# Performance work log

Measured on AMD Instinct MI355X. Metric: run time of the kernel, lower is better.

The kernel has to match this reference:

```python
import jax, jax.numpy as jnp
import numpy as np

N = 4096    # channels * n = 4 * 1024
N_IN = 1024
FC = 512


def ldr_layer(x, G, H, subd_A, subd_B, bias):
    """y = W x + bias, where W = sum_i K(A, g_i) K(B, h_i)^T and A, B are
    subdiagonal matrices with entries subd_A, subd_B (Krylov LDR fast multiply).

    Closed form: K(A, g)[i, j] = g[i-j] * c[i] / c[i-j] for i >= j (0 otherwise),
    with c = [1, cumprod(subd_A)]. This turns the multiply into FFT
    correlations/convolutions of length 2n instead of a dense n x n GEMM.
    x: (b, n); G, H: (r, n); subd_A, subd_B: (n-1,); bias: (n,).
    """
    n = x.shape[-1]
    one = jnp.ones((1,), x.dtype)
    c = jnp.concatenate([one, jnp.cumprod(subd_A)])   # (n,) cumulative subdiag products of A
    d = jnp.concatenate([one, jnp.cumprod(subd_B)])   # (n,)
    L = 2 * n
    q = H / d                                          # (r, n)
    gp = G / c                                         # (r, n)
    p = x * d                                          # (b, n)
    # u[b, r, j] = (K(B, h_r)^T x)[j] = sum_k q[r, k] * p[b, j + k]  (cross-correlation)
    Fp = jnp.fft.rfft(p, n=L)                          # (b, n+1)
    Fq = jnp.fft.rfft(q, n=L)                          # (r, n+1)
    u = jnp.fft.irfft(Fp[:, None] * jnp.conj(Fq)[None], n=L)[..., :n]  # (b, r, n)
    # out[b, i] = c[i] * sum_r (gp_r * u[b, r])_conv[i]  (causal convolution)
    Fg = jnp.fft.rfft(gp, n=L)                         # (r, n+1)
    Fu = jnp.fft.rfft(u, n=L)                          # (b, r, n+1)
    out = jnp.fft.irfft(jnp.einsum('rk,brk->bk', Fg, Fu), n=L)[:, :n]
    return c * out + bias


def setup_inputs() -> dict:
    key = jax.random.key(0)
    ks = jax.random.split(key, 14)
    std = 0.01  # params.init_stddev
    f32 = jnp.float32
    inp = {
        'x': jax.random.normal(ks[0], (128, N_IN), f32),
        'G1': std * jax.random.normal(ks[1], (48, N), f32),
        'H1': std * jax.random.normal(ks[2], (48, N), f32),
        'subd_A1': jnp.exp(0.01 * jax.random.normal(ks[3], (N - 1,), f32)),
        'subd_B1': jnp.exp(0.01 * jax.random.normal(ks[4], (N - 1,), f32)),
        'b1': std * jax.random.normal(ks[5], (N,), f32),
        'G2': std * jax.random.normal(ks[6], (16, N), f32),
        'H2': std * jax.random.normal(ks[7], (16, N), f32),
        'subd_A2': jnp.exp(0.01 * jax.random.normal(ks[8], (N - 1,), f32)),
        'subd_B2': jnp.exp(0.01 * jax.random.normal(ks[9], (N - 1,), f32)),
        'b2': std * jax.random.normal(ks[10], (N,), f32),
        'W_logits': jax.random.normal(ks[11], (10, FC), f32) / np.sqrt(FC).astype(np.float32),
        'b_logits': std * jax.random.normal(ks[12], (10,), f32),
    }
    return inp


def reference(x, G1, H1, subd_A1, subd_B1, b1, G2, H2, subd_A2, subd_B2, b2,
              W_logits, b_logits):
    bsz, n_in = x.shape
    xp = jnp.concatenate([x, jnp.zeros((bsz, N - n_in), x.dtype)], axis=-1)  # pad to channels*n
    h = jax.nn.relu(ldr_layer(xp, G1, H1, subd_A1, subd_B1, b1))
    h = jax.nn.relu(ldr_layer(h, G2, H2, subd_A2, subd_B2, b2))
    return h[:, :FC] @ W_logits.T + b_logits
```

## Files before the change

### kernel.cpp

```cpp
#include <hip/hip_runtime.h>
#include <hip/hip_bf16.h>

#define BATCH 128
#define NIN   1024
#define NFULL 4096
#define R1    48
#define R2    16
#define FCDIM 512
#define NOUT  10

#define WS_C1  0
#define WS_D1  4096
#define WS_C2  8192
#define WS_D2  12288
#define WS_P1  16384
#define WS_P2  (WS_P1 + BATCH*NIN)
#define WS_PT1 (WS_P2 + BATCH*NFULL)
#define WS_P2M (WS_PT1 + NIN*NFULL)
#define WS_CT1 (WS_P2M + FCDIM*NFULL)
#define WS_CT2 (WS_CT1 + 32*5120)
#define WS_VP1 (WS_CT2 + 16*4608)
#define WS_VP2 (WS_VP1 + 4*BATCH*NFULL)
#define WS_END (WS_VP2 + 32*BATCH*FCDIM)

#define NCH1 32
#define NCH2 16
#define CHROWS 32
#define CTLD1 5120
#define CTLD2 4608

typedef __attribute__((ext_vector_type(8))) short bf16x8;
typedef __attribute__((ext_vector_type(4))) float f32x4;

__device__ __forceinline__ unsigned short f2b(float f) {
    unsigned u = __builtin_bit_cast(unsigned, f);
    return (unsigned short)((u + 0x7fffu + ((u >> 16) & 1u)) >> 16);
}
__device__ __forceinline__ float b2f(unsigned short h) {
    unsigned u = ((unsigned)h) << 16;
    return __builtin_bit_cast(float, u);
}
#define MFMA16(a, b, c) __builtin_amdgcn_mfma_f32_16x16x32_bf16(a, b, c, 0, 0, 0)

__global__ void __launch_bounds__(256) prep_fused(
    const float* __restrict__ x, const float* __restrict__ sA1,
    const float* __restrict__ sB1, const float* __restrict__ sA2,
    const float* __restrict__ sB2, float* __restrict__ ws) {
    __shared__ float cd[4096];
    __shared__ float tot[256];
    int b = blockIdx.x, t = threadIdx.x;
    const float* src = (b == 0) ? sA1 : (b == 1) ? sB1 : (b == 2) ? sA2
                      : (b == 3) ? sB2 : sB1;
    float loc[16];
    float prod = 1.f;
#pragma unroll
    for (int u = 0; u < 16; ++u) {
        int idx = t * 16 + u;
        float e = (idx == 0) ? 1.f : src[idx - 1];
        prod *= e;
        loc[u] = prod;
    }
    tot[t] = prod;
    __syncthreads();
    for (int off = 1; off < 256; off <<= 1) {
        float v = (t >= off) ? tot[t - off] : 1.f;
        __syncthreads();
        tot[t] *= v;
        __syncthreads();
    }
    float excl = (t == 0) ? 1.f : tot[t - 1];
#pragma unroll
    for (int u = 0; u < 16; ++u) cd[t * 16 + u] = excl * loc[u];
    __syncthreads();

    if (b < 4) {
        float* dst = ws + (size_t)b * 4096;
#pragma unroll
        for (int u = 0; u < 16; ++u) { int i = t + u * 256; dst[i] = cd[i]; }
    } else {
        unsigned short* p1h = (unsigned short*)(ws + WS_P1);
        unsigned short* p1l = p1h + BATCH * NIN;
        int row0 = (b - 4) * 4;
#pragma unroll
        for (int u = 0; u < 16; ++u) {
            int lin = t + u * 256;
            int row = row0 + (lin >> 10), col = lin & 1023;
            float f = x[(size_t)row * NIN + col] * cd[col];
            unsigned short h = f2b(f);
            p1h[(size_t)row * NIN + col] = h;
            p1l[(size_t)row * NIN + col] = f2b(f - b2f(h));
        }
    }
}

__global__ void __launch_bounds__(256) gemm_rank_kernel(
    const float* __restrict__ H1, const float* __restrict__ G1,
    const float* __restrict__ G2, const float* __restrict__ H2,
    float* __restrict__ ws) {
    const int which = blockIdx.z;
    if (which == 1 && blockIdx.y >= 8) return;
    const float* A    = which == 0 ? H1 : G2;
    const float* B    = which == 0 ? G1 : H2;
    const float* divA = ws + (which == 0 ? WS_D1 : WS_C2);
    const float* divB = ws + (which == 0 ? WS_C1 : WS_D2);
    float* C          = ws + (which == 0 ? WS_PT1 : WS_P2M);
    const int Kr      = which == 0 ? R1 : R2;
    __shared__ float As[R1 * 68];
    __shared__ float Bs[R1 * 68];
    int tid = threadIdx.x;
    int tx = tid & 15, ty = tid >> 4;
    int n0 = blockIdx.x * 64;
    int m0 = blockIdx.y * 64;
    int nf4 = Kr * 16;
    for (int lin = tid; lin < nf4; lin += 256) {
        int r = lin >> 4, i4 = lin & 15;
        float4 va = *(const float4*)&A[(size_t)r * NFULL + m0 + i4 * 4];
        float4 da = *(const float4*)&divA[m0 + i4 * 4];
        va.x /= da.x; va.y /= da.y; va.z /= da.z; va.w /= da.w;
        *(float4*)&As[r * 68 + i4 * 4] = va;
        float4 vb = *(const float4*)&B[(size_t)r * NFULL + n0 + i4 * 4];
        float4 db = *(const float4*)&divB[n0 + i4 * 4];
        vb.x /= db.x; vb.y /= db.y; vb.z /= db.z; vb.w /= db.w;
        *(float4*)&Bs[r * 68 + i4 * 4] = vb;
    }
    __syncthreads();
    float acc[4][4] = {};
#pragma unroll 8
    for (int r = 0; r < Kr; ++r) {
        float4 a4 = *(const float4*)&As[r * 68 + ty * 4];
        float4 b4 = *(const float4*)&Bs[r * 68 + tx * 4];
        acc[0][0] += a4.x * b4.x; acc[0][1] += a4.x * b4.y;
        acc[0][2] += a4.x * b4.z; acc[0][3] += a4.x * b4.w;
        acc[1][0] += a4.y * b4.x; acc[1][1] += a4.y * b4.y;
        acc[1][2] += a4.y * b4.z; acc[1][3] += a4.y * b4.w;
        acc[2][0] += a4.z * b4.x; acc[2][1] += a4.z * b4.y;
        acc[2][2] += a4.z * b4.z; acc[2][3] += a4.z * b4.w;
        acc[3][0] += a4.w * b4.x; acc[3][1] += a4.w * b4.y;
        acc[3][2] += a4.w * b4.z; acc[3][3] += a4.w * b4.w;
    }
#pragma unroll
    for (int i = 0; i < 4; ++i) {
        int m = m0 + ty * 4 + i;
        *(float4*)&C[(size_t)m * NFULL + n0 + tx * 4] =
            make_float4(acc[i][0], acc[i][1], acc[i][2], acc[i][3]);
    }
}

__global__ void diag_scan_p1(float* __restrict__ ws) {
    const int which = blockIdx.z;
    const int nch   = which == 0 ? NCH1 : NCH2;
    if (blockIdx.y >= (unsigned)nch) return;
    float* P        = ws + (which == 0 ? WS_PT1 : WS_P2M);
    float* ctot     = ws + (which == 0 ? WS_CT1 : WS_CT2);
    const int R     = which == 0 ? NIN : FCDIM;
    const int nd    = R + NFULL - 1;
    const int ctld  = which == 0 ? CTLD1 : CTLD2;
    int t = blockIdx.x * 256 + threadIdx.x;
    if (t >= nd) return;
    int doff = t - (R - 1);
    int z = blockIdx.y;
    int m0 = z * CHROWS;
    int mlo = max(m0, -doff);
    int mhi = min(m0 + CHROWS, min(NFULL - doff, R));
    float run = 0.f;
    if (mlo < mhi) {
        float* p = P + (size_t)mlo * NFULL + (mlo + doff);
        const size_t step = NFULL + 1;
        int len = mhi - mlo;
        int s = 0;
        for (; s + 16 <= len; s += 16) {
            float v[16];
#pragma unroll
            for (int u = 0; u < 16; ++u) v[u] = p[u * step];
#pragma unroll
            for (int u = 0; u < 16; ++u) { run += v[u]; v[u] = run; }
#pragma unroll
            for (int u = 0; u < 16; ++u) p[u * step] = v[u];
            p += 16 * step;
        }
        for (; s < len; ++s) { float v = *p; run += v; *p = run; p += step; }
    }
    ctot[(size_t)z * ctld + t] = run;
}

__global__ void off_prefix(float* __restrict__ ws) {
    const int which = blockIdx.z;
    float* ct      = ws + (which == 0 ? WS_CT1 : WS_CT2);
    const int ctld = which == 0 ? CTLD1 : CTLD2;
    const int nch  = which == 0 ? NCH1 : NCH2;
    int t = blockIdx.x * 256 + threadIdx.x;
    if (t >= ctld) return;
    float run = 0.f;
    for (int z = 0; z < nch; ++z) {
        float v = ct[(size_t)z * ctld + t];
        ct[(size_t)z * ctld + t] = run;
        run += v;
    }
}

#define L1_LOADA(H0, H1, L0, L1v, KS) { \
    int kk_ = kbase + (KS) * 32 + 8 * g; \
    const unsigned short* pa_ = p1h + (size_t)(mq * 32 + lm) * NIN + kk_; \
    const unsigned short* pb_ = p1l + (size_t)(mq * 32 + lm) * NIN + kk_; \
    H0 = *(const bf16x8*)pa_;  H1 = *(const bf16x8*)(pa_ + 16 * NIN); \
    L0 = *(const bf16x8*)pb_;  L1v = *(const bf16x8*)(pb_ + 16 * NIN); }

#define L1_LOADS(KS) { \
    int kg_ = kbase + (KS) * 32 + 2 * k2; \
    const float* pr_ = P1 + (size_t)kg_ * NFULL + n0 + 2 * n2; \
    float2 va_ = *(const float2*)pr_; \
    float2 vb_ = *(const float2*)(pr_ + NFULL); \
    const float* orow_ = OFF1 + (size_t)(kg_ >> 5) * CTLD1 + (1023 + n0 + 2 * n2 - kg_); \
    float om_ = orow_[-1], oc_ = orow_[0], op_ = orow_[1]; \
    f00 = va_.x + oc_; f01 = va_.y + op_; f10 = vb_.x + om_; f11 = vb_.y + oc_; }

#define L1_WRITES() { \
    unsigned short h00_ = f2b(f00), h10_ = f2b(f10), h01_ = f2b(f01), h11_ = f2b(f11); \
    int a0_ = (2 * n2) * 20 + k2; \
    Bh[a0_]      = (unsigned)h00_ | ((unsigned)h10_ << 16); \
    Bh[a0_ + 20] = (unsigned)h01_ | ((unsigned)h11_ << 16); \
    Bl[a0_]      = (unsigned)f2b(f00 - b2f(h00_)) | ((unsigned)f2b(f10 - b2f(h10_)) << 16); \
    Bl[a0_ + 20] = (unsigned)f2b(f01 - b2f(h01_)) | ((unsigned)f2b(f11 - b2f(h11_)) << 16); }

#define L1_COMPUTE(H0, H1, L0, L1v) { \
    int nb_ = (nh * 32 + lm) * 20 + 4 * g; \
    uint4 uh0_ = *(const uint4*)&Bh[nb_];       uint4 ul0_ = *(const uint4*)&Bl[nb_]; \
    uint4 uh1_ = *(const uint4*)&Bh[nb_ + 320]; uint4 ul1_ = *(const uint4*)&Bl[nb_ + 320]; \
    bf16x8 bh0_ = __builtin_bit_cast(bf16x8, uh0_), bl0_ = __builtin_bit_cast(bf16x8, ul0_); \
    bf16x8 bh1_ = __builtin_bit_cast(bf16x8, uh1_), bl1_ = __builtin_bit_cast(bf16x8, ul1_); \
    acc00 = MFMA16(H0, bh0_, acc00); acc10 = MFMA16(H1, bh0_, acc10); \
    acc01 = MFMA16(H0, bh1_, acc01); acc11 = MFMA16(H1, bh1_, acc11); \
    acc00 = MFMA16(H0, bl0_, acc00); acc10 = MFMA16(H1, bl0_, acc10); \
    acc01 = MFMA16(H0, bl1_, acc01); acc11 = MFMA16(H1, bl1_, acc11); \
    acc00 = MFMA16(L0, bh0_, acc00); acc10 = MFMA16(L1v, bh0_, acc10); \
    acc01 = MFMA16(L0, bh1_, acc01); acc11 = MFMA16(L1v, bh1_, acc11); }

#define L1_STEP(CH0, CH1, CL0, CL1, NH0, NH1, NL0, NL1, KS, LAST) \
    __syncthreads(); \
    L1_WRITES(); \
    if (!(LAST)) { L1_LOADS((KS) + 1); L1_LOADA(NH0, NH1, NL0, NL1, (KS) + 1); } \
    __syncthreads(); \
    L1_COMPUTE(CH0, CH1, CL0, CL1);

__global__ void __launch_bounds__(512)
gemm2_l1_mfma(const float* __restrict__ P1, const float* __restrict__ OFF1,
              const unsigned short* __restrict__ p1h,
              const unsigned short* __restrict__ p1l, float* __restrict__ vp) {
    __shared__ unsigned Bh[64 * 20];
    __shared__ unsigned Bl[64 * 20];
    const int t = threadIdx.x;
    const int n0 = blockIdx.x * 64;
    const int kbase = blockIdx.z * 256;
    const int w = t >> 6, l = t & 63;
    const int mq = w >> 1, nh = w & 1;
    const int lm = l & 15, g = l >> 4;
    const int k2 = t >> 5, n2 = t & 31;

    f32x4 zero = {0.f, 0.f, 0.f, 0.f};
    f32x4 acc00 = zero, acc01 = zero, acc10 = zero, acc11 = zero;
    bf16x8 ahA0, ahA1, alA0, alA1, ahB0, ahB1, alB0, alB1;
    float f00, f01, f10, f11;

    L1_LOADS(0);
    L1_LOADA(ahA0, ahA1, alA0, alA1, 0);
    L1_STEP(ahA0, ahA1, alA0, alA1, ahB0, ahB1, alB0, alB1, 0, 0)
    L1_STEP(ahB0, ahB1, alB0, alB1, ahA0, ahA1, alA0, alA1, 1, 0)
    L1_STEP(ahA0, ahA1, alA0, alA1, ahB0, ahB1, alB0, alB1, 2, 0)
    L1_STEP(ahB0, ahB1, alB0, alB1, ahA0, ahA1, alA0, alA1, 3, 0)
    L1_STEP(ahA0, ahA1, alA0, alA1, ahB0, ahB1, alB0, alB1, 4, 0)
    L1_STEP(ahB0, ahB1, alB0, alB1, ahA0, ahA1, alA0, alA1, 5, 0)
    L1_STEP(ahA0, ahA1, alA0, alA1, ahB0, ahB1, alB0, alB1, 6, 0)
    L1_STEP(ahB0, ahB1, alB0, alB1, ahA0, ahA1, alA0, alA1, 7, 1)

    float* dst = vp + (size_t)blockIdx.z * BATCH * NFULL;
    int row0 = mq * 32 + 4 * g;
    int col0 = n0 + nh * 32 + lm;
#pragma unroll
    for (int r = 0; r < 4; ++r) {
        dst[(size_t)(row0 + r) * NFULL + col0]           = acc00[r];
        dst[(size_t)(row0 + r) * NFULL + col0 + 16]      = acc01[r];
        dst[(size_t)(row0 + 16 + r) * NFULL + col0]      = acc10[r];
        dst[(size_t)(row0 + 16 + r) * NFULL + col0 + 16] = acc11[r];
    }
}

__global__ void reduce_l1_kernel(const float* __restrict__ vp, const float* __restrict__ c1,
                                 const float* __restrict__ b1, const float* __restrict__ d2,
                                 unsigned short* __restrict__ p2h,
                                 unsigned short* __restrict__ p2l) {
    int idx4 = blockIdx.x * 256 + threadIdx.x;
    int base = idx4 * 4;
    int n = base & (NFULL - 1);
    float4 s = make_float4(0.f, 0.f, 0.f, 0.f);
#pragma unroll
    for (int z = 0; z < 4; ++z) {
        float4 v = *(const float4*)&vp[(size_t)z * BATCH * NFULL + base];
        s.x += v.x; s.y += v.y; s.z += v.z; s.w += v.w;
    }
    float4 cc = *(const float4*)&c1[n];
    float4 bb = *(const float4*)&b1[n];
    float4 dd = *(const float4*)&d2[n];
    float f[4];
    f[0] = fmaxf(cc.x * s.x + bb.x, 0.f) * dd.x;
    f[1] = fmaxf(cc.y * s.y + bb.y, 0.f) * dd.y;
    f[2] = fmaxf(cc.z * s.z + bb.z, 0.f) * dd.z;
    f[3] = fmaxf(cc.w * s.w + bb.w, 0.f) * dd.w;
    ushort4 hv, lv;
    unsigned short h;
    h = f2b(f[0]); hv.x = h; lv.x = f2b(f[0] - b2f(h));
    h = f2b(f[1]); hv.y = h; lv.y = f2b(f[1] - b2f(h));
    h = f2b(f[2]); hv.z = h; lv.z = f2b(f[2] - b2f(h));
    h = f2b(f[3]); hv.w = h; lv.w = f2b(f[3] - b2f(h));
    *(ushort4*)&p2h[base] = hv;
    *(ushort4*)&p2l[base] = lv;
}

__global__ void __launch_bounds__(512)
gemm2_l2_mfma(const unsigned short* __restrict__ p2h,
              const unsigned short* __restrict__ p2l,
              const float* __restrict__ M2, const float* __restrict__ OFF2,
              float* __restrict__ vp) {
    const int t = threadIdx.x;
    const int n0 = blockIdx.x * 64;
    const int kbase = blockIdx.z * 128;
    const int w = t >> 6, l = t & 63;
    const int mq = w >> 1, nh = w & 1;
    const int lm = l & 15, g = l >> 4;
    f32x4 zero = {0.f, 0.f, 0.f, 0.f};
    f32x4 acc00 = zero, acc01 = zero, acc10 = zero, acc11 = zero;
    const int nn0 = n0 + nh * 32 + lm;
    const int nn1 = nn0 + 16;
    const float* om0 = OFF2 + (size_t)(nn0 >> 5) * CTLD2 + (511 - nn0);
    const float* om1 = OFF2 + (size_t)(nn1 >> 5) * CTLD2 + (511 - nn1);
    const float* pm0 = M2 + (size_t)nn0 * NFULL;
    const float* pm1 = M2 + (size_t)nn1 * NFULL;

    float4 c0a, c0b, c1a, c1b, x0a, x0b, x1a, x1b;
    {
        int kk = kbase + 8 * g;
        c0a = *(const float4*)&pm0[kk]; c0b = *(const float4*)&pm0[kk + 4];
        c1a = *(const float4*)&pm1[kk]; c1b = *(const float4*)&pm1[kk + 4];
    }
#pragma unroll
    for (int ks = 0; ks < 4; ++ks) {
        int kk = kbase + ks * 32 + 8 * g;
        if (ks < 3) {
            int kn = kk + 32;
            x0a = *(const float4*)&pm0[kn]; x0b = *(const float4*)&pm0[kn + 4];
            x1a = *(const float4*)&pm1[kn]; x1b = *(const float4*)&pm1[kn + 4];
        }
        const unsigned short* pa = p2h + (size_t)(mq * 32 + lm) * NFULL + kk;
        const unsigned short* pb = p2l + (size_t)(mq * 32 + lm) * NFULL + kk;
        bf16x8 ah0 = *(const bf16x8*)pa, ah1 = *(const bf16x8*)(pa + 16 * NFULL);
        bf16x8 al0 = *(const bf16x8*)pb, al1 = *(const bf16x8*)(pb + 16 * NFULL);
        bf16x8 bh0, bl0, bh1, bl1;
        float m0v[8] = {c0a.x, c0a.y, c0a.z, c0a.w, c0b.x, c0b.y, c0b.z, c0b.w};
        float m1v[8] = {c1a.x, c1a.y, c1a.z, c1a.w, c1b.x, c1b.y, c1b.z, c1b.w};
#pragma unroll
        for (int r = 0; r < 8; ++r) {
            float f = m0v[r] + om0[kk + r];
            unsigned short h = f2b(f);
            bh0[r] = (short)h; bl0[r] = (short)f2b(f - b2f(h));
        }
#pragma unroll
        for (int r = 0; r < 8; ++r) {
            float f = m1v[r] + om1[kk + r];
            unsigned short h = f2b(f);
            bh1[r] = (short)h; bl1[r] = (short)f2b(f - b2f(h));
        }
        acc00 = MFMA16(ah0, bh0, acc00); acc10 = MFMA16(ah1, bh0, acc10);
        acc01 = MFMA16(ah0, bh1, acc01); acc11 = MFMA16(ah1, bh1, acc11);
        acc00 = MFMA16(ah0, bl0, acc00); acc10 = MFMA16(ah1, bl0, acc10);
        acc01 = MFMA16(ah0, bl1, acc01); acc11 = MFMA16(ah1, bl1, acc11);
        acc00 = MFMA16(al0, bh0, acc00); acc10 = MFMA16(al1, bh0, acc10);
        acc01 = MFMA16(al0, bh1, acc01); acc11 = MFMA16(al1, bh1, acc11);
        c0a = x0a; c0b = x0b; c1a = x1a; c1b = x1b;
    }
    float* dst = vp + (size_t)blockIdx.z * BATCH * FCDIM;
    int row0 = mq * 32 + 4 * g;
    int col0 = n0 + nh * 32 + lm;
#pragma unroll
    for (int r = 0; r < 4; ++r) {
        dst[(size_t)(row0 + r) * FCDIM + col0]           = acc00[r];
        dst[(size_t)(row0 + r) * FCDIM + col0 + 16]      = acc01[r];
        dst[(size_t)(row0 + 16 + r) * FCDIM + col0]      = acc10[r];
        dst[(size_t)(row0 + 16 + r) * FCDIM + col0 + 16] = acc11[r];
    }
}

__global__ void fused_out_kernel(const float* __restrict__ vp, const float* __restrict__ c2,
                                 const float* __restrict__ b2, const float* __restrict__ Wl,
                                 const float* __restrict__ bl, float* __restrict__ out) {
    __shared__ float h2s[FCDIM];
    int b = blockIdx.x, t = threadIdx.x;
    for (int col = t; col < FCDIM; col += 256) {
        float s = 0.f;
#pragma unroll
        for (int z = 0; z < 32; ++z)
            s += vp[((size_t)z * BATCH + b) * FCDIM + col];
        h2s[col] = fmaxf(c2[col] * s + b2[col], 0.f);
    }
    __syncthreads();
    int w = t >> 6, lane = t & 63;
    for (int o = w; o < NOUT; o += 4) {
        float s = 0.f;
#pragma unroll
        for (int i = lane; i < FCDIM; i += 64) s += h2s[i] * Wl[(size_t)o * FCDIM + i];
#pragma unroll
        for (int off = 32; off > 0; off >>= 1) s += __shfl_down(s, off);
        if (lane == 0) out[(size_t)b * NOUT + o] = s + bl[o];
    }
}

extern "C" void kernel_launch(void* const* d_in, const int* in_sizes, int n_in,
                              void* d_out, int out_size, void* d_ws, size_t ws_size,
                              hipStream_t stream) {
    const float* x   = (const float*)d_in[0];
    const float* G1  = (const float*)d_in[1];
    const float* H1  = (const float*)d_in[2];
    const float* sA1 = (const float*)d_in[3];
    const float* sB1 = (const float*)d_in[4];
    const float* b1  = (const float*)d_in[5];
    const float* G2  = (const float*)d_in[6];
    const float* H2  = (const float*)d_in[7];
    const float* sA2 = (const float*)d_in[8];
    const float* sB2 = (const float*)d_in[9];
    const float* b2  = (const float*)d_in[10];
    const float* Wl  = (const float*)d_in[11];
    const float* bl  = (const float*)d_in[12];
    float* out = (float*)d_out;
    float* ws = (float*)d_ws;
    (void)in_sizes; (void)n_in; (void)out_size; (void)ws_size;

    unsigned short* p1h = (unsigned short*)(ws + WS_P1);
    unsigned short* p1l = p1h + BATCH * NIN;
    unsigned short* p2h = (unsigned short*)(ws + WS_P2);
    unsigned short* p2l = p2h + BATCH * NFULL;

    prep_fused<<<36, 256, 0, stream>>>(x, sA1, sB1, sA2, sB2, ws);

    gemm_rank_kernel<<<dim3(64, 16, 2), 256, 0, stream>>>(H1, G1, G2, H2, ws);

    diag_scan_p1<<<dim3(20, NCH1, 2), 256, 0, stream>>>(ws);
    off_prefix<<<dim3(20, 1, 2), 256, 0, stream>>>(ws);

    gemm2_l1_mfma<<<dim3(64, 1, 4), 512, 0, stream>>>(ws + WS_PT1, ws + WS_CT1,
                                                      p1h, p1l, ws + WS_VP1);
    reduce_l1_kernel<<<512, 256, 0, stream>>>(ws + WS_VP1, ws + WS_C1, b1, ws + WS_D2,
                                              p2h, p2l);

    gemm2_l2_mfma<<<dim3(8, 1, 32), 512, 0, stream>>>(p2h, p2l, ws + WS_P2M,
                                                      ws + WS_CT2, ws + WS_VP2);

    fused_out_kernel<<<BATCH, 256, 0, stream>>>(ws + WS_VP2, ws + WS_C2, b2, Wl, bl, out);
}
```

Measured before the change: 75.37 us.

## Transpose layer-1 rank-sum matrix so GEMM reads B operand directly from global

The layer-1 low-rank product matrix is now stored transposed (output index major, input index minor), so the layer-1 MFMA GEMM can load its B operand straight from global rows with the diagonal offsets added in registers. This removes the LDS staging and the barriers of the old kernel. The diagonal scan chunking changes to match: 64 chunks of 64 rows for layer 1 and 8 chunks for layer 2. Divisions in the rank GEMM are replaced by multiplies with reciprocals precomputed in prep. The trade-off is strided diagonal scans over the new layout and more scalar offset loads per lane.

```diff
diff --git a/kernel.cpp b/kernel.cpp
--- a/kernel.cpp
+++ b/kernel.cpp
@@ -13,19 +13,22 @@
 #define WS_D1  4096
 #define WS_C2  8192
 #define WS_D2  12288
-#define WS_P1  16384
+#define WS_RC1 16384
+#define WS_RD1 20480
+#define WS_RC2 24576
+#define WS_RD2 28672
+#define WS_P1  32768
 #define WS_P2  (WS_P1 + BATCH*NIN)
 #define WS_PT1 (WS_P2 + BATCH*NFULL)
-#define WS_P2M (WS_PT1 + NIN*NFULL)
+#define WS_P2M (WS_PT1 + NFULL*NIN)
 #define WS_CT1 (WS_P2M + FCDIM*NFULL)
-#define WS_CT2 (WS_CT1 + 32*5120)
-#define WS_VP1 (WS_CT2 + 16*4608)
+#define WS_CT2 (WS_CT1 + 64*5120)
+#define WS_VP1 (WS_CT2 + 8*4608)
 #define WS_VP2 (WS_VP1 + 4*BATCH*NFULL)
 #define WS_END (WS_VP2 + 32*BATCH*FCDIM)
 
-#define NCH1 32
-#define NCH2 16
-#define CHROWS 32
+#define NCH1 64
+#define NCH2 8
 #define CTLD1 5120
 #define CTLD2 4608
 
@@ -75,8 +78,13 @@
 
     if (b < 4) {
         float* dst = ws + (size_t)b * 4096;
-#pragma unroll
-        for (int u = 0; u < 16; ++u) { int i = t + u * 256; dst[i] = cd[i]; }
+        float* rdst = ws + WS_RC1 + (size_t)b * 4096;
+#pragma unroll
+        for (int u = 0; u < 16; ++u) {
+            int i = t + u * 256;
+            dst[i] = cd[i];
+            rdst[i] = 1.f / cd[i];
+        }
     } else {
         unsigned short* p1h = (unsigned short*)(ws + WS_P1);
         unsigned short* p1l = p1h + BATCH * NIN;
@@ -94,33 +102,39 @@
 }
 
 __global__ void __launch_bounds__(256) gemm_rank_kernel(
-    const float* __restrict__ H1, const float* __restrict__ G1,
+    const float* __restrict__ G1, const float* __restrict__ H1,
     const float* __restrict__ G2, const float* __restrict__ H2,
     float* __restrict__ ws) {
-    const int which = blockIdx.z;
-    if (which == 1 && blockIdx.y >= 8) return;
-    const float* A    = which == 0 ? H1 : G2;
-    const float* B    = which == 0 ? G1 : H2;
-    const float* divA = ws + (which == 0 ? WS_D1 : WS_C2);
-    const float* divB = ws + (which == 0 ? WS_C1 : WS_D2);
-    float* C          = ws + (which == 0 ? WS_PT1 : WS_P2M);
-    const int Kr      = which == 0 ? R1 : R2;
+    int bid = blockIdx.x;
+    const float *A, *B, *mulA, *mulB;
+    float* C;
+    int Kr, ldc, m0, n0;
+    if (bid < 1024) {
+        A = G1; B = H1;
+        mulA = ws + WS_RC1; mulB = ws + WS_RD1;
+        C = ws + WS_PT1; Kr = R1; ldc = NIN;
+        n0 = (bid & 15) * 64; m0 = (bid >> 4) * 64;
+    } else {
+        int b = bid - 1024;
+        A = G2; B = H2;
+        mulA = ws + WS_RC2; mulB = ws + WS_RD2;
+        C = ws + WS_P2M; Kr = R2; ldc = NFULL;
+        n0 = (b & 63) * 64; m0 = (b >> 6) * 64;
+    }
     __shared__ float As[R1 * 68];
     __shared__ float Bs[R1 * 68];
     int tid = threadIdx.x;
     int tx = tid & 15, ty = tid >> 4;
-    int n0 = blockIdx.x * 64;
-    int m0 = blockIdx.y * 64;
     int nf4 = Kr * 16;
     for (int lin = tid; lin < nf4; lin += 256) {
         int r = lin >> 4, i4 = lin & 15;
         float4 va = *(const float4*)&A[(size_t)r * NFULL + m0 + i4 * 4];
-        float4 da = *(const float4*)&divA[m0 + i4 * 4];
-        va.x /= da.x; va.y /= da.y; va.z /= da.z; va.w /= da.w;
+        float4 da = *(const float4*)&mulA[m0 + i4 * 4];
+        va.x *= da.x; va.y *= da.y; va.z *= da.z; va.w *= da.w;
         *(float4*)&As[r * 68 + i4 * 4] = va;
         float4 vb = *(const float4*)&B[(size_t)r * NFULL + n0 + i4 * 4];
-        float4 db = *(const float4*)&divB[n0 + i4 * 4];
-        vb.x /= db.x; vb.y /= db.y; vb.z /= db.z; vb.w /= db.w;
+        float4 db = *(const float4*)&mulB[n0 + i4 * 4];
+        vb.x *= db.x; vb.y *= db.y; vb.z *= db.z; vb.w *= db.w;
         *(float4*)&Bs[r * 68 + i4 * 4] = vb;
     }
     __syncthreads();
@@ -141,7 +155,7 @@
 #pragma unroll
     for (int i = 0; i < 4; ++i) {
         int m = m0 + ty * 4 + i;
-        *(float4*)&C[(size_t)m * NFULL + n0 + tx * 4] =
+        *(float4*)&C[(size_t)m * ldc + n0 + tx * 4] =
             make_float4(acc[i][0], acc[i][1], acc[i][2], acc[i][3]);
     }
 }
@@ -152,21 +166,22 @@
     if (blockIdx.y >= (unsigned)nch) return;
     float* P        = ws + (which == 0 ? WS_PT1 : WS_P2M);
     float* ctot     = ws + (which == 0 ? WS_CT1 : WS_CT2);
-    const int R     = which == 0 ? NIN : FCDIM;
-    const int nd    = R + NFULL - 1;
+    const int R     = which == 0 ? NFULL : FCDIM;
+    const int C     = which == 0 ? NIN : NFULL;
+    const int nd    = R + C - 1;
     const int ctld  = which == 0 ? CTLD1 : CTLD2;
     int t = blockIdx.x * 256 + threadIdx.x;
     if (t >= nd) return;
     int doff = t - (R - 1);
     int z = blockIdx.y;
-    int m0 = z * CHROWS;
-    int mlo = max(m0, -doff);
-    int mhi = min(m0 + CHROWS, min(NFULL - doff, R));
+    int i0 = z * 64;
+    int ilo = max(i0, -doff);
+    int ihi = min(i0 + 64, min(C - doff, R));
     float run = 0.f;
-    if (mlo < mhi) {
-        float* p = P + (size_t)mlo * NFULL + (mlo + doff);
-        const size_t step = NFULL + 1;
-        int len = mhi - mlo;
+    if (ilo < ihi) {
+        float* p = P + (size_t)ilo * C + (ilo + doff);
+        const size_t step = (size_t)C + 1;
+        int len = ihi - ilo;
         int s = 0;
         for (; s + 16 <= len; s += 16) {
             float v[16];
@@ -198,80 +213,67 @@
     }
 }
 
-#define L1_LOADA(H0, H1, L0, L1v, KS) { \
-    int kk_ = kbase + (KS) * 32 + 8 * g; \
-    const unsigned short* pa_ = p1h + (size_t)(mq * 32 + lm) * NIN + kk_; \
-    const unsigned short* pb_ = p1l + (size_t)(mq * 32 + lm) * NIN + kk_; \
-    H0 = *(const bf16x8*)pa_;  H1 = *(const bf16x8*)(pa_ + 16 * NIN); \
-    L0 = *(const bf16x8*)pb_;  L1v = *(const bf16x8*)(pb_ + 16 * NIN); }
-
-#define L1_LOADS(KS) { \
-    int kg_ = kbase + (KS) * 32 + 2 * k2; \
-    const float* pr_ = P1 + (size_t)kg_ * NFULL + n0 + 2 * n2; \
-    float2 va_ = *(const float2*)pr_; \
-    float2 vb_ = *(const float2*)(pr_ + NFULL); \
-    const float* orow_ = OFF1 + (size_t)(kg_ >> 5) * CTLD1 + (1023 + n0 + 2 * n2 - kg_); \
-    float om_ = orow_[-1], oc_ = orow_[0], op_ = orow_[1]; \
-    f00 = va_.x + oc_; f01 = va_.y + op_; f10 = vb_.x + om_; f11 = vb_.y + oc_; }
-
-#define L1_WRITES() { \
-    unsigned short h00_ = f2b(f00), h10_ = f2b(f10), h01_ = f2b(f01), h11_ = f2b(f11); \
-    int a0_ = (2 * n2) * 20 + k2; \
-    Bh[a0_]      = (unsigned)h00_ | ((unsigned)h10_ << 16); \
-    Bh[a0_ + 20] = (unsigned)h01_ | ((unsigned)h11_ << 16); \
-    Bl[a0_]      = (unsigned)f2b(f00 - b2f(h00_)) | ((unsigned)f2b(f10 - b2f(h10_)) << 16); \
-    Bl[a0_ + 20] = (unsigned)f2b(f01 - b2f(h01_)) | ((unsigned)f2b(f11 - b2f(h11_)) << 16); }
-
-#define L1_COMPUTE(H0, H1, L0, L1v) { \
-    int nb_ = (nh * 32 + lm) * 20 + 4 * g; \
-    uint4 uh0_ = *(const uint4*)&Bh[nb_];       uint4 ul0_ = *(const uint4*)&Bl[nb_]; \
-    uint4 uh1_ = *(const uint4*)&Bh[nb_ + 320]; uint4 ul1_ = *(const uint4*)&Bl[nb_ + 320]; \
-    bf16x8 bh0_ = __builtin_bit_cast(bf16x8, uh0_), bl0_ = __builtin_bit_cast(bf16x8, ul0_); \
-    bf16x8 bh1_ = __builtin_bit_cast(bf16x8, uh1_), bl1_ = __builtin_bit_cast(bf16x8, ul1_); \
-    acc00 = MFMA16(H0, bh0_, acc00); acc10 = MFMA16(H1, bh0_, acc10); \
-    acc01 = MFMA16(H0, bh1_, acc01); acc11 = MFMA16(H1, bh1_, acc11); \
-    acc00 = MFMA16(H0, bl0_, acc00); acc10 = MFMA16(H1, bl0_, acc10); \
-    acc01 = MFMA16(H0, bl1_, acc01); acc11 = MFMA16(H1, bl1_, acc11); \
-    acc00 = MFMA16(L0, bh0_, acc00); acc10 = MFMA16(L1v, bh0_, acc10); \
-    acc01 = MFMA16(L0, bh1_, acc01); acc11 = MFMA16(L1v, bh1_, acc11); }
-
-#define L1_STEP(CH0, CH1, CL0, CL1, NH0, NH1, NL0, NL1, KS, LAST) \
-    __syncthreads(); \
-    L1_WRITES(); \
-    if (!(LAST)) { L1_LOADS((KS) + 1); L1_LOADA(NH0, NH1, NL0, NL1, (KS) + 1); } \
-    __syncthreads(); \
-    L1_COMPUTE(CH0, CH1, CL0, CL1);
-
 __global__ void __launch_bounds__(512)
-gemm2_l1_mfma(const float* __restrict__ P1, const float* __restrict__ OFF1,
-              const unsigned short* __restrict__ p1h,
-              const unsigned short* __restrict__ p1l, float* __restrict__ vp) {
-    __shared__ unsigned Bh[64 * 20];
-    __shared__ unsigned Bl[64 * 20];
+gemm2_l1_mfma(const unsigned short* __restrict__ p1h,
+              const unsigned short* __restrict__ p1l,
+              const float* __restrict__ S1, const float* __restrict__ OFF1,
+              float* __restrict__ vp) {
     const int t = threadIdx.x;
     const int n0 = blockIdx.x * 64;
     const int kbase = blockIdx.z * 256;
     const int w = t >> 6, l = t & 63;
     const int mq = w >> 1, nh = w & 1;
     const int lm = l & 15, g = l >> 4;
-    const int k2 = t >> 5, n2 = t & 31;
-
     f32x4 zero = {0.f, 0.f, 0.f, 0.f};
     f32x4 acc00 = zero, acc01 = zero, acc10 = zero, acc11 = zero;
-    bf16x8 ahA0, ahA1, alA0, alA1, ahB0, ahB1, alB0, alB1;
-    float f00, f01, f10, f11;
-
-    L1_LOADS(0);
-    L1_LOADA(ahA0, ahA1, alA0, alA1, 0);
-    L1_STEP(ahA0, ahA1, alA0, alA1, ahB0, ahB1, alB0, alB1, 0, 0)
-    L1_STEP(ahB0, ahB1, alB0, alB1, ahA0, ahA1, alA0, alA1, 1, 0)
-    L1_STEP(ahA0, ahA1, alA0, alA1, ahB0, ahB1, alB0, alB1, 2, 0)
-    L1_STEP(ahB0, ahB1, alB0, alB1, ahA0, ahA1, alA0, alA1, 3, 0)
-    L1_STEP(ahA0, ahA1, alA0, alA1, ahB0, ahB1, alB0, alB1, 4, 0)
-    L1_STEP(ahB0, ahB1, alB0, alB1, ahA0, ahA1, alA0, alA1, 5, 0)
-    L1_STEP(ahA0, ahA1, alA0, alA1, ahB0, ahB1, alB0, alB1, 6, 0)
-    L1_STEP(ahB0, ahB1, alB0, alB1, ahA0, ahA1, alA0, alA1, 7, 1)
-
+    const int nn0 = n0 + nh * 32 + lm;
+    const int nn1 = nn0 + 16;
+    const float* om0 = OFF1 + (size_t)(nn0 >> 6) * CTLD1 + (4095 - nn0);
+    const float* om1 = OFF1 + (size_t)(nn1 >> 6) * CTLD1 + (4095 - nn1);
+    const float* pm0 = S1 + (size_t)nn0 * NIN;
+    const float* pm1 = S1 + (size_t)nn1 * NIN;
+
+    float4 c0a, c0b, c1a, c1b, x0a, x0b, x1a, x1b;
+    {
+        int kk = kbase + 8 * g;
+        c0a = *(const float4*)&pm0[kk]; c0b = *(const float4*)&pm0[kk + 4];
+        c1a = *(const float4*)&pm1[kk]; c1b = *(const float4*)&pm1[kk + 4];
+    }
+#pragma unroll
+    for (int ks = 0; ks < 8; ++ks) {
+        int kk = kbase + ks * 32 + 8 * g;
+        if (ks < 7) {
+            int kn = kk + 32;
+            x0a = *(const float4*)&pm0[kn]; x0b = *(const float4*)&pm0[kn + 4];
+            x1a = *(const float4*)&pm1[kn]; x1b = *(const float4*)&pm1[kn + 4];
+        }
+        const unsigned short* pa = p1h + (size_t)(mq * 32 + lm) * NIN + kk;
+        const unsigned short* pb = p1l + (size_t)(mq * 32 + lm) * NIN + kk;
+        bf16x8 ah0 = *(const bf16x8*)pa, ah1 = *(const bf16x8*)(pa + 16 * NIN);
+        bf16x8 al0 = *(const bf16x8*)pb, al1 = *(const bf16x8*)(pb + 16 * NIN);
+        bf16x8 bh0, bl0, bh1, bl1;
+        float m0v[8] = {c0a.x, c0a.y, c0a.z, c0a.w, c0b.x, c0b.y, c0b.z, c0b.w};
+        float m1v[8] = {c1a.x, c1a.y, c1a.z, c1a.w, c1b.x, c1b.y, c1b.z, c1b.w};
+#pragma unroll
+        for (int r = 0; r < 8; ++r) {
+            float f = m0v[r] + om0[kk + r];
+            unsigned short h = f2b(f);
+            bh0[r] = (short)h; bl0[r] = (short)f2b(f - b2f(h));
+        }
+#pragma unroll
+        for (int r = 0; r < 8; ++r) {
+            float f = m1v[r] + om1[kk + r];
+            unsigned short h = f2b(f);
+            bh1[r] = (short)h; bl1[r] = (short)f2b(f - b2f(h));
+        }
+        acc00 = MFMA16(ah0, bh0, acc00); acc10 = MFMA16(ah1, bh0, acc10);
+        acc01 = MFMA16(ah0, bh1, acc01); acc11 = MFMA16(ah1, bh1, acc11);
+        acc00 = MFMA16(ah0, bl0, acc00); acc10 = MFMA16(ah1, bl0, acc10);
+        acc01 = MFMA16(ah0, bl1, acc01); acc11 = MFMA16(ah1, bl1, acc11);
+        acc00 = MFMA16(al0, bh0, acc00); acc10 = MFMA16(al1, bh0, acc10);
+        acc01 = MFMA16(al0, bh1, acc01); acc11 = MFMA16(al1, bh1, acc11);
+        c0a = x0a; c0b = x0b; c1a = x1a; c1b = x1b;
+    }
     float* dst = vp + (size_t)blockIdx.z * BATCH * NFULL;
     int row0 = mq * 32 + 4 * g;
     int col0 = n0 + nh * 32 + lm;
@@ -330,8 +332,8 @@
     f32x4 acc00 = zero, acc01 = zero, acc10 = zero, acc11 = zero;
     const int nn0 = n0 + nh * 32 + lm;
     const int nn1 = nn0 + 16;
-    const float* om0 = OFF2 + (size_t)(nn0 >> 5) * CTLD2 + (511 - nn0);
-    const float* om1 = OFF2 + (size_t)(nn1 >> 5) * CTLD2 + (511 - nn1);
+    const float* om0 = OFF2 + (size_t)(nn0 >> 6) * CTLD2 + (511 - nn0);
+    const float* om1 = OFF2 + (size_t)(nn1 >> 6) * CTLD2 + (511 - nn1);
     const float* pm0 = M2 + (size_t)nn0 * NFULL;
     const float* pm1 = M2 + (size_t)nn1 * NFULL;
 
@@ -439,13 +441,13 @@
 
     prep_fused<<<36, 256, 0, stream>>>(x, sA1, sB1, sA2, sB2, ws);
 
-    gemm_rank_kernel<<<dim3(64, 16, 2), 256, 0, stream>>>(H1, G1, G2, H2, ws);
+    gemm_rank_kernel<<<1536, 256, 0, stream>>>(G1, H1, G2, H2, ws);
 
     diag_scan_p1<<<dim3(20, NCH1, 2), 256, 0, stream>>>(ws);
     off_prefix<<<dim3(20, 1, 2), 256, 0, stream>>>(ws);
 
-    gemm2_l1_mfma<<<dim3(64, 1, 4), 512, 0, stream>>>(ws + WS_PT1, ws + WS_CT1,
-                                                      p1h, p1l, ws + WS_VP1);
+    gemm2_l1_mfma<<<dim3(64, 1, 4), 512, 0, stream>>>(p1h, p1l, ws + WS_PT1,
+                                                      ws + WS_CT1, ws + WS_VP1);
     reduce_l1_kernel<<<512, 256, 0, stream>>>(ws + WS_VP1, ws + WS_C1, b1, ws + WS_D2,
                                               p2h, p2l);
 
```

New measurement: 93.42 us. 24.0% more time.
